# Performance work log

Hardware: AMD Instinct MI355X
Metric: run time of the kernel (lower is better)

## Reference

```python
import jax, jax.numpy as jnp
import numpy as np
from jax import lax

TOP_K = 2

def setup_inputs() -> dict:
    key = jax.random.key(0)
    k0, k1, k2, k3, k4 = jax.random.split(key, 5)
    B, S, H, I, E = 2, 2048, 1024, 2048, 8
    hidden_states = jax.random.normal(k0, (B, S, H), dtype=jnp.float32)
    Wr = jax.random.normal(k1, (H, E), dtype=jnp.float32) * 0.02   # router (no bias)
    Wg = jax.random.normal(k2, (E, H, I), dtype=jnp.float32) * 0.02  # gate proj per expert
    Wu = jax.random.normal(k3, (E, H, I), dtype=jnp.float32) * 0.02  # up proj per expert
    Wd = jax.random.normal(k4, (E, I, H), dtype=jnp.float32) * 0.02  # down proj per expert
    return {"hidden_states": hidden_states, "Wr": Wr, "Wg": Wg, "Wu": Wu, "Wd": Wd}

def reference(hidden_states, Wr, Wg, Wu, Wd):
    B, S, H = hidden_states.shape
    x = hidden_states.reshape(B * S, H)            # [T,H]
    routes = x @ Wr                                # [T,E]
    T, E = routes.shape
    top_vals, top_idx = lax.top_k(routes, TOP_K)   # [T,K]
    top_w = jax.nn.softmax(top_vals, axis=-1)      # softmax over selected k only
    # scatter softmaxed scores back to dense [T,E] (zeros elsewhere)
    w = jnp.zeros((T, E), dtype=x.dtype).at[jnp.arange(T)[:, None], top_idx].set(top_w)
    # dense per-expert SwiGLU; zero routing weight => zero contribution (same math
    # as the original gather/scatter expert loop)
    gate = jnp.einsum('th,ehi->tei', x, Wg)        # [T,E,I]
    up = jnp.einsum('th,ehi->tei', x, Wu)          # [T,E,I]
    expert_out = jnp.einsum('tei,eih->teh', jax.nn.silu(gate) * up, Wd)  # [T,E,H]
    out = jnp.einsum('te,teh->th', w, expert_out)  # weighted combine
    return out.reshape(B, S, H)
```

## Files before the change

### kernel.cpp

```cpp
#include <hip/hip_runtime.h>
#include <stdint.h>

#define T_TOK 4096
#define H_DIM 1024
#define E_NUM 8
#define I_DIM 2048
#define CAP   9216
#define MAXTILES 72

typedef float f32x4 __attribute__((ext_vector_type(4)));
typedef __bf16 bf16x8 __attribute__((ext_vector_type(8)));
typedef unsigned short u16x8 __attribute__((ext_vector_type(8)));
typedef unsigned short u16x4 __attribute__((ext_vector_type(4)));

__device__ __forceinline__ unsigned short f2bf(float f) {
    union { float f; unsigned int u; } v; v.f = f;
    unsigned int u = v.u;
    return (unsigned short)((u + 0x7fffu + ((u >> 16) & 1u)) >> 16);
}
__device__ __forceinline__ float bf2f(unsigned short s) {
    union { unsigned int u; float f; } v; v.u = ((unsigned int)s) << 16; return v.f;
}

__device__ __forceinline__ void async16(const unsigned short* g, unsigned short* l) {
    __builtin_amdgcn_global_load_lds(
        (const __attribute__((address_space(1))) unsigned int*)g,
        (__attribute__((address_space(3))) unsigned int*)l,
        16, 0, 0);
}

__global__ __launch_bounds__(256)
void router_kernel(const float* __restrict__ x, const float* __restrict__ Wr,
                   unsigned short* __restrict__ xb, int* __restrict__ topidx,
                   float* __restrict__ topw) {
    int wv = threadIdx.x >> 6, lane = threadIdx.x & 63;
    int t = blockIdx.x * 4 + wv;
    const float* xrow = x + (size_t)t * H_DIM + lane * 16;
    const float* wrow = Wr + (size_t)lane * 16 * E_NUM;
    float acc[E_NUM];
#pragma unroll
    for (int e = 0; e < E_NUM; e++) acc[e] = 0.f;
    unsigned short xo[16];
#pragma unroll
    for (int c = 0; c < 4; c++) {
        f32x4 xv = *(const f32x4*)(xrow + c * 4);
#pragma unroll
        for (int k = 0; k < 4; k++) {
            float v = xv[k];
            xo[c * 4 + k] = f2bf(v);
            const float* wr = wrow + (c * 4 + k) * E_NUM;
#pragma unroll
            for (int e = 0; e < E_NUM; e++) acc[e] += v * wr[e];
        }
    }
    unsigned short* xbp = xb + (size_t)t * H_DIM + lane * 16;
    *(u16x8*)xbp = *(u16x8*)xo;
    *(u16x8*)(xbp + 8) = *(u16x8*)(xo + 8);
#pragma unroll
    for (int m = 1; m < 64; m <<= 1) {
#pragma unroll
        for (int e = 0; e < E_NUM; e++) acc[e] += __shfl_xor(acc[e], m);
    }
    if (lane == 0) {
        float v0 = -1e30f; int i0 = 0;
#pragma unroll
        for (int e = 0; e < E_NUM; e++) { if (acc[e] > v0) { v0 = acc[e]; i0 = e; } }
        float v1 = -1e30f; int i1 = 0;
#pragma unroll
        for (int e = 0; e < E_NUM; e++) { if (e != i0 && acc[e] > v1) { v1 = acc[e]; i1 = e; } }
        float e1 = __expf(v1 - v0);
        float s = 1.f + e1;
        topidx[t * 2 + 0] = i0; topidx[t * 2 + 1] = i1;
        topw[t * 2 + 0] = 1.f / s; topw[t * 2 + 1] = e1 / s;
    }
}

__global__ __launch_bounds__(256)
void offsets_pad_kernel(const int* __restrict__ topidx, int* __restrict__ padded,
                        int* __restrict__ offs, int* __restrict__ tile_e,
                        int* __restrict__ tile_base, int* __restrict__ ntiles,
                        int* __restrict__ list_tok, float* __restrict__ list_w) {
    __shared__ int sc[E_NUM], sp[E_NUM], so[E_NUM + 1], snt;
    __shared__ int ste[MAXTILES], stb[MAXTILES];
    __shared__ int whist[4][E_NUM];
    int tid = threadIdx.x;
    int wv = tid >> 6, lane = tid & 63;
    int cnt[E_NUM];
#pragma unroll
    for (int e = 0; e < E_NUM; e++) cnt[e] = 0;
    for (int a = tid; a < T_TOK * 2; a += 256) {
        int e = topidx[a];
#pragma unroll
        for (int k = 0; k < E_NUM; k++) cnt[k] += (e == k) ? 1 : 0;
    }
#pragma unroll
    for (int m = 1; m < 64; m <<= 1)
#pragma unroll
        for (int e = 0; e < E_NUM; e++) cnt[e] += __shfl_xor(cnt[e], m);
    if (lane == 0) {
#pragma unroll
        for (int e = 0; e < E_NUM; e++) whist[wv][e] = cnt[e];
    }
    if (tid < MAXTILES) { ste[tid] = 0; stb[tid] = 0; }
    __syncthreads();
    if (tid == 0) {
        int off = 0, nt_e[E_NUM];
        for (int e = 0; e < E_NUM; e++) {
            sc[e] = whist[0][e] + whist[1][e] + whist[2][e] + whist[3][e];
            so[e] = off;
            int p = (sc[e] + 127) & ~127;
            sp[e] = p; nt_e[e] = p >> 7; off += p;
        }
        so[E_NUM] = off;
        int t2 = 0;
        for (int r = 0; r < MAXTILES; r++)
            for (int e = 0; e < E_NUM; e++)
                if (r < nt_e[e]) { ste[t2] = e; stb[t2] = so[e] + (r << 7); t2++; }
        snt = t2;
    }
    __syncthreads();
    if (tid < E_NUM) { padded[tid] = sp[tid]; offs[tid] = so[tid]; }
    if (tid == E_NUM) { offs[E_NUM] = so[E_NUM]; ntiles[0] = snt; }
    if (tid < MAXTILES) { tile_e[tid] = ste[tid]; tile_base[tid] = stb[tid]; }
#pragma unroll
    for (int e = 0; e < E_NUM; e++)
        for (int pos = sc[e] + tid; pos < sp[e]; pos += 256) {
            list_tok[so[e] + pos] = 0;
            list_w[so[e] + pos] = 0.f;
        }
}

__global__ __launch_bounds__(256)
void scatter_kernel(const int* __restrict__ topidx, const float* __restrict__ topw,
                    const int* __restrict__ offs, int* __restrict__ cursors,
                    int* __restrict__ list_tok, float* __restrict__ list_w,
                    int* __restrict__ slot_of) {
    __shared__ int lcnt[E_NUM], gbase[E_NUM];
    int tid = threadIdx.x;
    if (tid < E_NUM) lcnt[tid] = 0;
    __syncthreads();
    int a = blockIdx.x * 256 + tid;
    int e = topidx[a];
    int lpos = atomicAdd(&lcnt[e], 1);
    __syncthreads();
    if (tid < E_NUM) gbase[tid] = atomicAdd(&cursors[tid], lcnt[tid]);
    __syncthreads();
    int slot = offs[e] + gbase[e] + lpos;
    list_tok[slot] = a >> 1;
    list_w[slot]   = topw[a];
    slot_of[a]     = slot;
}

__global__ __launch_bounds__(256)
void transpose_all(const float* __restrict__ Wg, const float* __restrict__ Wu,
                   const float* __restrict__ Wd, unsigned short* __restrict__ wgT,
                   unsigned short* __restrict__ wuT, unsigned short* __restrict__ wdT) {
    __shared__ float tile[64][69];
    int z = blockIdx.z, bx = blockIdx.x, by = blockIdx.y;
    const float* in; unsigned short* out;
    int R, C, c0, r0;
    size_t mat = (size_t)H_DIM * I_DIM;
    if (z < 16) {
        int e = z & 7;
        in  = (z < 8 ? Wg : Wu) + (size_t)e * mat;
        out = (z < 8 ? wgT : wuT) + (size_t)e * mat;
        R = H_DIM; C = I_DIM;
        c0 = bx * 64; r0 = by * 64;
    } else {
        int e = z - 16;
        in  = Wd + (size_t)e * mat;
        out = wdT + (size_t)e * mat;
        R = I_DIM; C = H_DIM;
        c0 = by * 64; r0 = bx * 64;
    }
    int tid = threadIdx.x;
    int lc = (tid & 15) * 4, lr = tid >> 4;
#pragma unroll
    for (int j = 0; j < 64; j += 16) {
        f32x4 v = *(const f32x4*)(in + (size_t)(r0 + lr + j) * C + c0 + lc);
        tile[lr + j][lc + 0] = v[0]; tile[lr + j][lc + 1] = v[1];
        tile[lr + j][lc + 2] = v[2]; tile[lr + j][lc + 3] = v[3];
    }
    __syncthreads();
    int r8 = (tid & 7) * 8;
#pragma unroll
    for (int cc = 0; cc < 64; cc += 32) {
        int c = cc + (tid >> 3);
        u16x8 u;
#pragma unroll
        for (int j = 0; j < 8; j++) u[j] = f2bf(tile[r8 + j][c]);
        *(u16x8*)(out + (size_t)(c0 + c) * R + r0 + r8) = u;
    }
}

__global__ __launch_bounds__(256, 3)
void gemm_gateup(const unsigned short* __restrict__ xb, const unsigned short* __restrict__ wgT,
                 const unsigned short* __restrict__ wuT, const int* __restrict__ list_tok,
                 const float* __restrict__ list_w,
                 const int* __restrict__ tile_e, const int* __restrict__ tile_base,
                 const int* __restrict__ ntiles, unsigned short* __restrict__ hbuf) {
    int tile = blockIdx.x;
    if (tile >= ntiles[0]) return;
    int e = tile_e[tile], base = tile_base[tile], nt = blockIdx.y;

    __shared__ unsigned short As[128 * 64];
    __shared__ unsigned short Bgs[64 * 64];
    __shared__ unsigned short Bus[64 * 64];
    __shared__ int toks[128];
    __shared__ float wsh[128];

    int tid = threadIdx.x;
    if (tid < 128) { toks[tid] = list_tok[base + tid]; wsh[tid] = list_w[base + tid]; }
    __syncthreads();

    const unsigned short* wg = wgT + ((size_t)e * I_DIM + (size_t)nt * 64) * H_DIM;
    const unsigned short* wu = wuT + ((size_t)e * I_DIM + (size_t)nt * 64) * H_DIM;

    int wv = tid >> 6, lane = tid & 63;
    int sr = lane >> 3, sc = lane & 7, gc = sc ^ sr;

    const unsigned short* ag[4]; const unsigned short* bgg[2]; const unsigned short* bug[2];
    int lbA[4], lbB[2];
#pragma unroll
    for (int i = 0; i < 4; i++) {
        int row = wv * 32 + i * 8 + sr;
        ag[i]  = xb + (size_t)toks[row] * H_DIM + gc * 8;
        lbA[i] = (wv * 32 + i * 8) * 64;
    }
#pragma unroll
    for (int i = 0; i < 2; i++) {
        int row = wv * 16 + i * 8 + sr;
        bgg[i] = wg + (size_t)row * H_DIM + gc * 8;
        bug[i] = wu + (size_t)row * H_DIM + gc * 8;
        lbB[i] = (wv * 16 + i * 8) * 64;
    }

    f32x4 accg[4][2], accu[4][2];
    f32x4 z = {0.f, 0.f, 0.f, 0.f};
#pragma unroll
    for (int i = 0; i < 4; i++)
#pragma unroll
        for (int j = 0; j < 2; j++) { accg[i][j] = z; accu[i][j] = z; }

    int wm = (wv >> 1) * 64, wn = (wv & 1) * 32;
    int l16 = lane & 15, quad = lane >> 4;

    for (int kb = 0; kb < H_DIM; kb += 64) {
#pragma unroll
        for (int i = 0; i < 4; i++) async16(ag[i] + kb, &As[lbA[i]]);
#pragma unroll
        for (int i = 0; i < 2; i++) {
            async16(bgg[i] + kb, &Bgs[lbB[i]]);
            async16(bug[i] + kb, &Bus[lbB[i]]);
        }
        __syncthreads();
#pragma unroll
        for (int ks = 0; ks < 2; ks++) {
            bf16x8 af[4], bg4[2], bu4[2];
#pragma unroll
            for (int i = 0; i < 4; i++) {
                int row = wm + i * 16 + l16;
                int pos = ((ks * 4 + quad) ^ (row & 7)) * 8;
                af[i] = *(const bf16x8*)(&As[row * 64 + pos]);
            }
#pragma unroll
            for (int j = 0; j < 2; j++) {
                int row = wn + j * 16 + l16;
                int pos = ((ks * 4 + quad) ^ (row & 7)) * 8;
                bg4[j] = *(const bf16x8*)(&Bgs[row * 64 + pos]);
                bu4[j] = *(const bf16x8*)(&Bus[row * 64 + pos]);
            }
#pragma unroll
            for (int i = 0; i < 4; i++)
#pragma unroll
                for (int j = 0; j < 2; j++) {
                    accg[i][j] = __builtin_amdgcn_mfma_f32_16x16x32_bf16(af[i], bg4[j], accg[i][j], 0, 0, 0);
                    accu[i][j] = __builtin_amdgcn_mfma_f32_16x16x32_bf16(af[i], bu4[j], accu[i][j], 0, 0, 0);
                }
        }
        __syncthreads();
    }
#pragma unroll
    for (int i = 0; i < 4; i++) {
#pragma unroll
        for (int r = 0; r < 4; r++) {
            int row = wm + i * 16 + quad * 4 + r;
            float wgt = wsh[row];
            size_t hb = (size_t)(base + row) * I_DIM + (size_t)nt * 64 + wn;
#pragma unroll
            for (int j = 0; j < 2; j++) {
                float g = accg[i][j][r];
                float u = accu[i][j][r];
                float sig = 1.f / (1.f + __expf(-g));
                hbuf[hb + j * 16 + l16] = f2bf(g * sig * u * wgt);
            }
        }
    }
}

__global__ __launch_bounds__(256, 4)
void gemm_down(const unsigned short* __restrict__ hbuf, const unsigned short* __restrict__ wdT,
               const int* __restrict__ tile_e, const int* __restrict__ tile_base,
               const int* __restrict__ ntiles, unsigned short* __restrict__ dbuf) {
    int tile = blockIdx.x;
    if (tile >= ntiles[0]) return;
    int e = tile_e[tile], base = tile_base[tile], nt = blockIdx.y;

    __shared__ unsigned short As[128 * 64];
    __shared__ unsigned short Bs[64 * 64];

    int tid = threadIdx.x;
    const unsigned short* wd = wdT + ((size_t)e * H_DIM + (size_t)nt * 64) * I_DIM;

    int wv = tid >> 6, lane = tid & 63;
    int sr = lane >> 3, sc = lane & 7, gc = sc ^ sr;

    const unsigned short* ag[4]; const unsigned short* bg[2];
    int lbA[4], lbB[2];
#pragma unroll
    for (int i = 0; i < 4; i++) {
        int row = wv * 32 + i * 8 + sr;
        ag[i] = hbuf + (size_t)(base + row) * I_DIM + gc * 8;
        lbA[i] = (wv * 32 + i * 8) * 64;
    }
#pragma unroll
    for (int i = 0; i < 2; i++) {
        int row = wv * 16 + i * 8 + sr;
        bg[i] = wd + (size_t)row * I_DIM + gc * 8;
        lbB[i] = (wv * 16 + i * 8) * 64;
    }

    f32x4 acc[4][2];
    f32x4 z = {0.f, 0.f, 0.f, 0.f};
#pragma unroll
    for (int i = 0; i < 4; i++)
#pragma unroll
        for (int j = 0; j < 2; j++) acc[i][j] = z;

    int wm = (wv >> 1) * 64, wn = (wv & 1) * 32;
    int l16 = lane & 15, quad = lane >> 4;

    for (int kb = 0; kb < I_DIM; kb += 64) {
#pragma unroll
        for (int i = 0; i < 4; i++) async16(ag[i] + kb, &As[lbA[i]]);
#pragma unroll
        for (int i = 0; i < 2; i++) async16(bg[i] + kb, &Bs[lbB[i]]);
        __syncthreads();
#pragma unroll
        for (int ks = 0; ks < 2; ks++) {
            bf16x8 af[4], bf4[2];
#pragma unroll
            for (int i = 0; i < 4; i++) {
                int row = wm + i * 16 + l16;
                int pos = ((ks * 4 + quad) ^ (row & 7)) * 8;
                af[i] = *(const bf16x8*)(&As[row * 64 + pos]);
            }
#pragma unroll
            for (int j = 0; j < 2; j++) {
                int row = wn + j * 16 + l16;
                int pos = ((ks * 4 + quad) ^ (row & 7)) * 8;
                bf4[j] = *(const bf16x8*)(&Bs[row * 64 + pos]);
            }
#pragma unroll
            for (int i = 0; i < 4; i++)
#pragma unroll
                for (int j = 0; j < 2; j++)
                    acc[i][j] = __builtin_amdgcn_mfma_f32_16x16x32_bf16(af[i], bf4[j], acc[i][j], 0, 0, 0);
        }
        __syncthreads();
    }
#pragma unroll
    for (int i = 0; i < 4; i++) {
#pragma unroll
        for (int r = 0; r < 4; r++) {
            int row = wm + i * 16 + quad * 4 + r;
            unsigned short* orow = dbuf + (size_t)(base + row) * H_DIM + (size_t)nt * 64 + wn;
#pragma unroll
            for (int j = 0; j < 2; j++)
                orow[j * 16 + l16] = f2bf(acc[i][j][r]);
        }
    }
}

__global__ __launch_bounds__(256)
void combine_kernel(const unsigned short* __restrict__ dbuf, const int* __restrict__ slot_of,
                    float* __restrict__ out) {
    int t = blockIdx.x;
    int s0 = slot_of[2 * t], s1 = slot_of[2 * t + 1];
    int i = threadIdx.x;
    u16x4 a = *(const u16x4*)(dbuf + (size_t)s0 * H_DIM + i * 4);
    u16x4 b = *(const u16x4*)(dbuf + (size_t)s1 * H_DIM + i * 4);
    f32x4 o;
#pragma unroll
    for (int k = 0; k < 4; k++) o[k] = bf2f(a[k]) + bf2f(b[k]);
    *(f32x4*)(out + (size_t)t * H_DIM + i * 4) = o;
}

extern "C" void kernel_launch(void* const* d_in, const int* in_sizes, int n_in,
                              void* d_out, int out_size, void* d_ws, size_t ws_size,
                              hipStream_t stream) {
    const float* x  = (const float*)d_in[0];
    const float* Wr = (const float*)d_in[1];
    const float* Wg = (const float*)d_in[2];
    const float* Wu = (const float*)d_in[3];
    const float* Wd = (const float*)d_in[4];
    float* out = (float*)d_out;
    char* ws = (char*)d_ws;

    size_t off = 0;
    unsigned short* xb   = (unsigned short*)(ws + off); off += (size_t)T_TOK * H_DIM * 2;
    unsigned short* wgT  = (unsigned short*)(ws + off); off += (size_t)E_NUM * H_DIM * I_DIM * 2;
    unsigned short* wuT  = (unsigned short*)(ws + off); off += (size_t)E_NUM * H_DIM * I_DIM * 2;
    unsigned short* wdT  = (unsigned short*)(ws + off); off += (size_t)E_NUM * H_DIM * I_DIM * 2;
    unsigned short* hbuf = (unsigned short*)(ws + off); off += (size_t)CAP * I_DIM * 2;
    unsigned short* dbuf = (unsigned short*)(ws + off); off += (size_t)CAP * H_DIM * 2;
    int*   topidx  = (int*)(ws + off);   off += (size_t)T_TOK * 2 * 4;
    float* topw    = (float*)(ws + off); off += (size_t)T_TOK * 2 * 4;
    int*   slot_of = (int*)(ws + off);   off += (size_t)T_TOK * 2 * 4;
    int*   meta    = (int*)(ws + off);   off += 1024;
    int*   cursors = meta + 8;
    int*   padded  = meta + 16;
    int*   offs    = meta + 24;
    int*   ntiles  = meta + 33;
    int*   tile_e  = meta + 64;
    int*   tile_b  = meta + 136;
    int*   list_tok = (int*)(ws + off);  off += (size_t)CAP * 4;
    float* list_w   = (float*)(ws + off); off += (size_t)CAP * 4;

    hipMemsetAsync(meta, 0, 64, stream);

    router_kernel<<<T_TOK / 4, 256, 0, stream>>>(x, Wr, xb, topidx, topw);
    transpose_all<<<dim3(32, 16, 24), 256, 0, stream>>>(Wg, Wu, Wd, wgT, wuT, wdT);
    offsets_pad_kernel<<<1, 256, 0, stream>>>(topidx, padded, offs, tile_e, tile_b, ntiles, list_tok, list_w);
    scatter_kernel<<<(T_TOK * 2) / 256, 256, 0, stream>>>(topidx, topw, offs, cursors, list_tok, list_w, slot_of);
    gemm_gateup<<<dim3(MAXTILES, I_DIM / 64), 256, 0, stream>>>(xb, wgT, wuT, list_tok, list_w, tile_e, tile_b, ntiles, hbuf);
    gemm_down<<<dim3(MAXTILES, H_DIM / 64), 256, 0, stream>>>(hbuf, wdT, tile_e, tile_b, ntiles, dbuf);
    combine_kernel<<<T_TOK, 256, 0, stream>>>(dbuf, slot_of, out);
}
```

Baseline: 407.2 us.

## Double-buffer LDS tiles in both expert GEMMs with async prefetch overlap

Converts the gate/up and down GEMM main loops to a two-stage LDS pipeline. The next K-tile is issued with async global-to-LDS loads while the current tile is computed, and partial vmcnt waits plus raw s_barrier calls replace the two __syncthreads per iteration. This aims to hide global load latency behind MFMA work. In exchange LDS use doubles and the launch-bounds occupancy hints drop by one (3->2 and 4->3). The token and weight shared arrays are also removed in favour of direct global reads.

```diff
diff --git a/kernel.cpp b/kernel.cpp
--- a/kernel.cpp
+++ b/kernel.cpp
@@ -193,7 +193,7 @@
     }
 }
 
-__global__ __launch_bounds__(256, 3)
+__global__ __launch_bounds__(256, 2)
 void gemm_gateup(const unsigned short* __restrict__ xb, const unsigned short* __restrict__ wgT,
                  const unsigned short* __restrict__ wuT, const int* __restrict__ list_tok,
                  const float* __restrict__ list_w,
@@ -203,16 +203,11 @@
     if (tile >= ntiles[0]) return;
     int e = tile_e[tile], base = tile_base[tile], nt = blockIdx.y;
 
-    __shared__ unsigned short As[128 * 64];
-    __shared__ unsigned short Bgs[64 * 64];
-    __shared__ unsigned short Bus[64 * 64];
-    __shared__ int toks[128];
-    __shared__ float wsh[128];
+    __shared__ unsigned short As[2][128 * 64];
+    __shared__ unsigned short Bgs[2][64 * 64];
+    __shared__ unsigned short Bus[2][64 * 64];
 
     int tid = threadIdx.x;
-    if (tid < 128) { toks[tid] = list_tok[base + tid]; wsh[tid] = list_w[base + tid]; }
-    __syncthreads();
-
     const unsigned short* wg = wgT + ((size_t)e * I_DIM + (size_t)nt * 64) * H_DIM;
     const unsigned short* wu = wuT + ((size_t)e * I_DIM + (size_t)nt * 64) * H_DIM;
 
@@ -224,7 +219,7 @@
 #pragma unroll
     for (int i = 0; i < 4; i++) {
         int row = wv * 32 + i * 8 + sr;
-        ag[i]  = xb + (size_t)toks[row] * H_DIM + gc * 8;
+        ag[i]  = xb + (size_t)list_tok[base + row] * H_DIM + gc * 8;
         lbA[i] = (wv * 32 + i * 8) * 64;
     }
 #pragma unroll
@@ -245,47 +240,68 @@
     int wm = (wv >> 1) * 64, wn = (wv & 1) * 32;
     int l16 = lane & 15, quad = lane >> 4;
 
-    for (int kb = 0; kb < H_DIM; kb += 64) {
-#pragma unroll
-        for (int i = 0; i < 4; i++) async16(ag[i] + kb, &As[lbA[i]]);
-#pragma unroll
-        for (int i = 0; i < 2; i++) {
-            async16(bgg[i] + kb, &Bgs[lbB[i]]);
-            async16(bug[i] + kb, &Bus[lbB[i]]);
-        }
-        __syncthreads();
-#pragma unroll
-        for (int ks = 0; ks < 2; ks++) {
-            bf16x8 af[4], bg4[2], bu4[2];
-#pragma unroll
-            for (int i = 0; i < 4; i++) {
-                int row = wm + i * 16 + l16;
-                int pos = ((ks * 4 + quad) ^ (row & 7)) * 8;
-                af[i] = *(const bf16x8*)(&As[row * 64 + pos]);
-            }
-#pragma unroll
-            for (int j = 0; j < 2; j++) {
-                int row = wn + j * 16 + l16;
-                int pos = ((ks * 4 + quad) ^ (row & 7)) * 8;
-                bg4[j] = *(const bf16x8*)(&Bgs[row * 64 + pos]);
-                bu4[j] = *(const bf16x8*)(&Bus[row * 64 + pos]);
-            }
-#pragma unroll
-            for (int i = 0; i < 4; i++)
-#pragma unroll
-                for (int j = 0; j < 2; j++) {
-                    accg[i][j] = __builtin_amdgcn_mfma_f32_16x16x32_bf16(af[i], bg4[j], accg[i][j], 0, 0, 0);
-                    accu[i][j] = __builtin_amdgcn_mfma_f32_16x16x32_bf16(af[i], bu4[j], accu[i][j], 0, 0, 0);
-                }
-        }
-        __syncthreads();
-    }
+#define STAGE_GU(b, kb) do {                                              \
+    _Pragma("unroll")                                                     \
+    for (int i_ = 0; i_ < 4; i_++) async16(ag[i_] + (kb), &As[b][lbA[i_]]); \
+    _Pragma("unroll")                                                     \
+    for (int i_ = 0; i_ < 2; i_++) {                                      \
+        async16(bgg[i_] + (kb), &Bgs[b][lbB[i_]]);                        \
+        async16(bug[i_] + (kb), &Bus[b][lbB[i_]]);                        \
+    }                                                                     \
+} while (0)
+
+#define COMPUTE_GU(b) do {                                                \
+    _Pragma("unroll")                                                     \
+    for (int ks = 0; ks < 2; ks++) {                                      \
+        bf16x8 af[4], bg4[2], bu4[2];                                     \
+        _Pragma("unroll")                                                 \
+        for (int i_ = 0; i_ < 4; i_++) {                                  \
+            int row = wm + i_ * 16 + l16;                                 \
+            int pos = ((ks * 4 + quad) ^ (row & 7)) * 8;                  \
+            af[i_] = *(const bf16x8*)(&As[b][row * 64 + pos]);            \
+        }                                                                 \
+        _Pragma("unroll")                                                 \
+        for (int j_ = 0; j_ < 2; j_++) {                                  \
+            int row = wn + j_ * 16 + l16;                                 \
+            int pos = ((ks * 4 + quad) ^ (row & 7)) * 8;                  \
+            bg4[j_] = *(const bf16x8*)(&Bgs[b][row * 64 + pos]);          \
+            bu4[j_] = *(const bf16x8*)(&Bus[b][row * 64 + pos]);          \
+        }                                                                 \
+        _Pragma("unroll")                                                 \
+        for (int i_ = 0; i_ < 4; i_++)                                    \
+            _Pragma("unroll")                                             \
+            for (int j_ = 0; j_ < 2; j_++) {                              \
+                accg[i_][j_] = __builtin_amdgcn_mfma_f32_16x16x32_bf16(af[i_], bg4[j_], accg[i_][j_], 0, 0, 0); \
+                accu[i_][j_] = __builtin_amdgcn_mfma_f32_16x16x32_bf16(af[i_], bu4[j_], accu[i_][j_], 0, 0, 0); \
+            }                                                             \
+    }                                                                     \
+} while (0)
+
+    STAGE_GU(0, 0);
+    int cur = 0;
+    for (int t = 0; t < (H_DIM / 64) - 1; t++) {
+        STAGE_GU(cur ^ 1, (t + 1) * 64);
+        asm volatile("s_waitcnt vmcnt(8)" ::: "memory");
+        __builtin_amdgcn_s_barrier();
+        __builtin_amdgcn_sched_barrier(0);
+        COMPUTE_GU(cur);
+        __builtin_amdgcn_sched_barrier(0);
+        __builtin_amdgcn_s_barrier();
+        cur ^= 1;
+    }
+    asm volatile("s_waitcnt vmcnt(0)" ::: "memory");
+    __builtin_amdgcn_s_barrier();
+    __builtin_amdgcn_sched_barrier(0);
+    COMPUTE_GU(cur);
+#undef STAGE_GU
+#undef COMPUTE_GU
+
 #pragma unroll
     for (int i = 0; i < 4; i++) {
 #pragma unroll
         for (int r = 0; r < 4; r++) {
             int row = wm + i * 16 + quad * 4 + r;
-            float wgt = wsh[row];
+            float wgt = list_w[base + row];
             size_t hb = (size_t)(base + row) * I_DIM + (size_t)nt * 64 + wn;
 #pragma unroll
             for (int j = 0; j < 2; j++) {
@@ -298,7 +314,7 @@
     }
 }
 
-__global__ __launch_bounds__(256, 4)
+__global__ __launch_bounds__(256, 3)
 void gemm_down(const unsigned short* __restrict__ hbuf, const unsigned short* __restrict__ wdT,
                const int* __restrict__ tile_e, const int* __restrict__ tile_base,
                const int* __restrict__ ntiles, unsigned short* __restrict__ dbuf) {
@@ -306,8 +322,8 @@
     if (tile >= ntiles[0]) return;
     int e = tile_e[tile], base = tile_base[tile], nt = blockIdx.y;
 
-    __shared__ unsigned short As[128 * 64];
-    __shared__ unsigned short Bs[64 * 64];
+    __shared__ unsigned short As[2][128 * 64];
+    __shared__ unsigned short Bs[2][64 * 64];
 
     int tid = threadIdx.x;
     const unsigned short* wd = wdT + ((size_t)e * H_DIM + (size_t)nt * 64) * I_DIM;
@@ -340,35 +356,56 @@
     int wm = (wv >> 1) * 64, wn = (wv & 1) * 32;
     int l16 = lane & 15, quad = lane >> 4;
 
-    for (int kb = 0; kb < I_DIM; kb += 64) {
-#pragma unroll
-        for (int i = 0; i < 4; i++) async16(ag[i] + kb, &As[lbA[i]]);
-#pragma unroll
-        for (int i = 0; i < 2; i++) async16(bg[i] + kb, &Bs[lbB[i]]);
-        __syncthreads();
-#pragma unroll
-        for (int ks = 0; ks < 2; ks++) {
-            bf16x8 af[4], bf4[2];
-#pragma unroll
-            for (int i = 0; i < 4; i++) {
-                int row = wm + i * 16 + l16;
-                int pos = ((ks * 4 + quad) ^ (row & 7)) * 8;
-                af[i] = *(const bf16x8*)(&As[row * 64 + pos]);
-            }
-#pragma unroll
-            for (int j = 0; j < 2; j++) {
-                int row = wn + j * 16 + l16;
-                int pos = ((ks * 4 + quad) ^ (row & 7)) * 8;
-                bf4[j] = *(const bf16x8*)(&Bs[row * 64 + pos]);
-            }
-#pragma unroll
-            for (int i = 0; i < 4; i++)
-#pragma unroll
-                for (int j = 0; j < 2; j++)
-                    acc[i][j] = __builtin_amdgcn_mfma_f32_16x16x32_bf16(af[i], bf4[j], acc[i][j], 0, 0, 0);
-        }
-        __syncthreads();
-    }
+#define STAGE_D(b, kb) do {                                               \
+    _Pragma("unroll")                                                     \
+    for (int i_ = 0; i_ < 4; i_++) async16(ag[i_] + (kb), &As[b][lbA[i_]]); \
+    _Pragma("unroll")                                                     \
+    for (int i_ = 0; i_ < 2; i_++) async16(bg[i_] + (kb), &Bs[b][lbB[i_]]); \
+} while (0)
+
+#define COMPUTE_D(b) do {                                                 \
+    _Pragma("unroll")                                                     \
+    for (int ks = 0; ks < 2; ks++) {                                      \
+        bf16x8 af[4], bf4[2];                                             \
+        _Pragma("unroll")                                                 \
+        for (int i_ = 0; i_ < 4; i_++) {                                  \
+            int row = wm + i_ * 16 + l16;                                 \
+            int pos = ((ks * 4 + quad) ^ (row & 7)) * 8;                  \
+            af[i_] = *(const bf16x8*)(&As[b][row * 64 + pos]);            \
+        }                                                                 \
+        _Pragma("unroll")                                                 \
+        for (int j_ = 0; j_ < 2; j_++) {                                  \
+            int row = wn + j_ * 16 + l16;                                 \
+            int pos = ((ks * 4 + quad) ^ (row & 7)) * 8;                  \
+            bf4[j_] = *(const bf16x8*)(&Bs[b][row * 64 + pos]);           \
+        }                                                                 \
+        _Pragma("unroll")                                                 \
+        for (int i_ = 0; i_ < 4; i_++)                                    \
+            _Pragma("unroll")                                             \
+            for (int j_ = 0; j_ < 2; j_++)                                \
+                acc[i_][j_] = __builtin_amdgcn_mfma_f32_16x16x32_bf16(af[i_], bf4[j_], acc[i_][j_], 0, 0, 0); \
+    }                                                                     \
+} while (0)
+
+    STAGE_D(0, 0);
+    int cur = 0;
+    for (int t = 0; t < (I_DIM / 64) - 1; t++) {
+        STAGE_D(cur ^ 1, (t + 1) * 64);
+        asm volatile("s_waitcnt vmcnt(6)" ::: "memory");
+        __builtin_amdgcn_s_barrier();
+        __builtin_amdgcn_sched_barrier(0);
+        COMPUTE_D(cur);
+        __builtin_amdgcn_sched_barrier(0);
+        __builtin_amdgcn_s_barrier();
+        cur ^= 1;
+    }
+    asm volatile("s_waitcnt vmcnt(0)" ::: "memory");
+    __builtin_amdgcn_s_barrier();
+    __builtin_amdgcn_sched_barrier(0);
+    COMPUTE_D(cur);
+#undef STAGE_D
+#undef COMPUTE_D
+
 #pragma unroll
     for (int i = 0; i < 4; i++) {
 #pragma unroll
```

Result: slower. 441.5 us (+8.4%).

## Fuse scatter into offsets kernel and widen down-proj tile to 128 columns

Applied to the files above, without the earlier changes.

Merges the offsets/padding and scatter kernels into one single-block kernel that assigns slots with shared-memory atomics, which removes a launch and the memset of the global cursors. The down-projection GEMM now uses a 128x128 output tile instead of 128x64, doubling per-wave accumulators so each A tile loaded from hbuf is reused across more columns. The grid is halved and launch bounds drop to 3 blocks per CU to leave room for the extra registers and LDS. The single-block scatter serialises about 8K assignments on one CU, and the larger tile lowers occupancy and block count.

```diff
diff --git a/kernel.cpp b/kernel.cpp
--- a/kernel.cpp
+++ b/kernel.cpp
@@ -76,13 +76,15 @@
 }
 
 __global__ __launch_bounds__(256)
-void offsets_pad_kernel(const int* __restrict__ topidx, int* __restrict__ padded,
-                        int* __restrict__ offs, int* __restrict__ tile_e,
-                        int* __restrict__ tile_base, int* __restrict__ ntiles,
-                        int* __restrict__ list_tok, float* __restrict__ list_w) {
+void offsets_scatter_kernel(const int* __restrict__ topidx, const float* __restrict__ topw,
+                            int* __restrict__ tile_e, int* __restrict__ tile_base,
+                            int* __restrict__ ntiles,
+                            int* __restrict__ list_tok, float* __restrict__ list_w,
+                            int* __restrict__ slot_of) {
     __shared__ int sc[E_NUM], sp[E_NUM], so[E_NUM + 1], snt;
     __shared__ int ste[MAXTILES], stb[MAXTILES];
     __shared__ int whist[4][E_NUM];
+    __shared__ int scur[E_NUM];
     int tid = threadIdx.x;
     int wv = tid >> 6, lane = tid & 63;
     int cnt[E_NUM];
@@ -101,6 +103,7 @@
 #pragma unroll
         for (int e = 0; e < E_NUM; e++) whist[wv][e] = cnt[e];
     }
+    if (tid < E_NUM) scur[tid] = 0;
     if (tid < MAXTILES) { ste[tid] = 0; stb[tid] = 0; }
     __syncthreads();
     if (tid == 0) {
@@ -119,36 +122,22 @@
         snt = t2;
     }
     __syncthreads();
-    if (tid < E_NUM) { padded[tid] = sp[tid]; offs[tid] = so[tid]; }
-    if (tid == E_NUM) { offs[E_NUM] = so[E_NUM]; ntiles[0] = snt; }
+    if (tid == 0) ntiles[0] = snt;
     if (tid < MAXTILES) { tile_e[tid] = ste[tid]; tile_base[tid] = stb[tid]; }
+    for (int a = tid; a < T_TOK * 2; a += 256) {
+        int e = topidx[a];
+        int pos = atomicAdd(&scur[e], 1);
+        int slot = so[e] + pos;
+        list_tok[slot] = a >> 1;
+        list_w[slot]   = topw[a];
+        slot_of[a]     = slot;
+    }
 #pragma unroll
     for (int e = 0; e < E_NUM; e++)
         for (int pos = sc[e] + tid; pos < sp[e]; pos += 256) {
             list_tok[so[e] + pos] = 0;
             list_w[so[e] + pos] = 0.f;
         }
-}
-
-__global__ __launch_bounds__(256)
-void scatter_kernel(const int* __restrict__ topidx, const float* __restrict__ topw,
-                    const int* __restrict__ offs, int* __restrict__ cursors,
-                    int* __restrict__ list_tok, float* __restrict__ list_w,
-                    int* __restrict__ slot_of) {
-    __shared__ int lcnt[E_NUM], gbase[E_NUM];
-    int tid = threadIdx.x;
-    if (tid < E_NUM) lcnt[tid] = 0;
-    __syncthreads();
-    int a = blockIdx.x * 256 + tid;
-    int e = topidx[a];
-    int lpos = atomicAdd(&lcnt[e], 1);
-    __syncthreads();
-    if (tid < E_NUM) gbase[tid] = atomicAdd(&cursors[tid], lcnt[tid]);
-    __syncthreads();
-    int slot = offs[e] + gbase[e] + lpos;
-    list_tok[slot] = a >> 1;
-    list_w[slot]   = topw[a];
-    slot_of[a]     = slot;
 }
 
 __global__ __launch_bounds__(256)
@@ -298,7 +287,7 @@
     }
 }
 
-__global__ __launch_bounds__(256, 4)
+__global__ __launch_bounds__(256, 3)
 void gemm_down(const unsigned short* __restrict__ hbuf, const unsigned short* __restrict__ wdT,
                const int* __restrict__ tile_e, const int* __restrict__ tile_base,
                const int* __restrict__ ntiles, unsigned short* __restrict__ dbuf) {
@@ -307,48 +296,44 @@
     int e = tile_e[tile], base = tile_base[tile], nt = blockIdx.y;
 
     __shared__ unsigned short As[128 * 64];
-    __shared__ unsigned short Bs[64 * 64];
+    __shared__ unsigned short Bs[128 * 64];
 
     int tid = threadIdx.x;
-    const unsigned short* wd = wdT + ((size_t)e * H_DIM + (size_t)nt * 64) * I_DIM;
+    const unsigned short* wd = wdT + ((size_t)e * H_DIM + (size_t)nt * 128) * I_DIM;
 
     int wv = tid >> 6, lane = tid & 63;
     int sr = lane >> 3, sc = lane & 7, gc = sc ^ sr;
 
-    const unsigned short* ag[4]; const unsigned short* bg[2];
-    int lbA[4], lbB[2];
+    const unsigned short* ag[4]; const unsigned short* bg[4];
+    int lb[4];
 #pragma unroll
     for (int i = 0; i < 4; i++) {
         int row = wv * 32 + i * 8 + sr;
         ag[i] = hbuf + (size_t)(base + row) * I_DIM + gc * 8;
-        lbA[i] = (wv * 32 + i * 8) * 64;
-    }
-#pragma unroll
-    for (int i = 0; i < 2; i++) {
-        int row = wv * 16 + i * 8 + sr;
         bg[i] = wd + (size_t)row * I_DIM + gc * 8;
-        lbB[i] = (wv * 16 + i * 8) * 64;
-    }
-
-    f32x4 acc[4][2];
+        lb[i] = (wv * 32 + i * 8) * 64;
+    }
+
+    f32x4 acc[4][4];
     f32x4 z = {0.f, 0.f, 0.f, 0.f};
 #pragma unroll
     for (int i = 0; i < 4; i++)
 #pragma unroll
-        for (int j = 0; j < 2; j++) acc[i][j] = z;
-
-    int wm = (wv >> 1) * 64, wn = (wv & 1) * 32;
+        for (int j = 0; j < 4; j++) acc[i][j] = z;
+
+    int wm = (wv >> 1) * 64, wn = (wv & 1) * 64;
     int l16 = lane & 15, quad = lane >> 4;
 
     for (int kb = 0; kb < I_DIM; kb += 64) {
 #pragma unroll
-        for (int i = 0; i < 4; i++) async16(ag[i] + kb, &As[lbA[i]]);
-#pragma unroll
-        for (int i = 0; i < 2; i++) async16(bg[i] + kb, &Bs[lbB[i]]);
+        for (int i = 0; i < 4; i++) {
+            async16(ag[i] + kb, &As[lb[i]]);
+            async16(bg[i] + kb, &Bs[lb[i]]);
+        }
         __syncthreads();
 #pragma unroll
         for (int ks = 0; ks < 2; ks++) {
-            bf16x8 af[4], bf4[2];
+            bf16x8 af[4], bf4[4];
 #pragma unroll
             for (int i = 0; i < 4; i++) {
                 int row = wm + i * 16 + l16;
@@ -356,7 +341,7 @@
                 af[i] = *(const bf16x8*)(&As[row * 64 + pos]);
             }
 #pragma unroll
-            for (int j = 0; j < 2; j++) {
+            for (int j = 0; j < 4; j++) {
                 int row = wn + j * 16 + l16;
                 int pos = ((ks * 4 + quad) ^ (row & 7)) * 8;
                 bf4[j] = *(const bf16x8*)(&Bs[row * 64 + pos]);
@@ -364,7 +349,7 @@
 #pragma unroll
             for (int i = 0; i < 4; i++)
 #pragma unroll
-                for (int j = 0; j < 2; j++)
+                for (int j = 0; j < 4; j++)
                     acc[i][j] = __builtin_amdgcn_mfma_f32_16x16x32_bf16(af[i], bf4[j], acc[i][j], 0, 0, 0);
         }
         __syncthreads();
@@ -374,9 +359,9 @@
 #pragma unroll
         for (int r = 0; r < 4; r++) {
             int row = wm + i * 16 + quad * 4 + r;
-            unsigned short* orow = dbuf + (size_t)(base + row) * H_DIM + (size_t)nt * 64 + wn;
-#pragma unroll
-            for (int j = 0; j < 2; j++)
+            unsigned short* orow = dbuf + (size_t)(base + row) * H_DIM + (size_t)nt * 128 + wn;
+#pragma unroll
+            for (int j = 0; j < 4; j++)
                 orow[j * 16 + l16] = f2bf(acc[i][j][r]);
         }
     }
@@ -418,22 +403,16 @@
     float* topw    = (float*)(ws + off); off += (size_t)T_TOK * 2 * 4;
     int*   slot_of = (int*)(ws + off);   off += (size_t)T_TOK * 2 * 4;
     int*   meta    = (int*)(ws + off);   off += 1024;
-    int*   cursors = meta + 8;
-    int*   padded  = meta + 16;
-    int*   offs    = meta + 24;
     int*   ntiles  = meta + 33;
     int*   tile_e  = meta + 64;
     int*   tile_b  = meta + 136;
     int*   list_tok = (int*)(ws + off);  off += (size_t)CAP * 4;
     float* list_w   = (float*)(ws + off); off += (size_t)CAP * 4;
 
-    hipMemsetAsync(meta, 0, 64, stream);
-
     router_kernel<<<T_TOK / 4, 256, 0, stream>>>(x, Wr, xb, topidx, topw);
     transpose_all<<<dim3(32, 16, 24), 256, 0, stream>>>(Wg, Wu, Wd, wgT, wuT, wdT);
-    offsets_pad_kernel<<<1, 256, 0, stream>>>(topidx, padded, offs, tile_e, tile_b, ntiles, list_tok, list_w);
-    scatter_kernel<<<(T_TOK * 2) / 256, 256, 0, stream>>>(topidx, topw, offs, cursors, list_tok, list_w, slot_of);
+    offsets_scatter_kernel<<<1, 256, 0, stream>>>(topidx, topw, tile_e, tile_b, ntiles, list_tok, list_w, slot_of);
     gemm_gateup<<<dim3(MAXTILES, I_DIM / 64), 256, 0, stream>>>(xb, wgT, wuT, list_tok, list_w, tile_e, tile_b, ntiles, hbuf);
-    gemm_down<<<dim3(MAXTILES, H_DIM / 64), 256, 0, stream>>>(hbuf, wdT, tile_e, tile_b, ntiles, dbuf);
+    gemm_down<<<dim3(MAXTILES, H_DIM / 128), 256, 0, stream>>>(hbuf, wdT, tile_e, tile_b, ntiles, dbuf);
     combine_kernel<<<T_TOK, 256, 0, stream>>>(dbuf, slot_of, out);
 }
```

Result: slower. 416.4 us (+2.3%).
